# Performance work log

Measured on AMD Instinct MI355X. Metric: run time of the kernel, lower is better.

## Reference

```python
import jax, jax.numpy as jnp
import numpy as np

N_NODES = 65536
N_EDGES = 1048576


def gcn_conv(x, edge_index, edge_weight, W, b):
    """PyG GCNConv: h = D^{-1/2}(A+I)D^{-1/2} x W + b, scatter to target (edge_index[1])."""
    n = x.shape[0]
    row, col = edge_index[0], edge_index[1]
    loop = jnp.arange(n)
    row_f = jnp.concatenate([row, loop])
    col_f = jnp.concatenate([col, loop])
    w_f = jnp.concatenate([edge_weight, jnp.ones((n,), dtype=x.dtype)])
    deg = jax.ops.segment_sum(w_f, col_f, num_segments=n)
    dis = jnp.where(deg > 0, jax.lax.rsqrt(jnp.where(deg > 0, deg, 1.0)), 0.0)
    norm = dis[row_f] * w_f * dis[col_f]  # [E+N]
    h = x @ W  # [N, out]
    msg = h[row_f] * norm[:, None]  # gather + scale
    out = jax.ops.segment_sum(msg, col_f, num_segments=n)
    return out + b


def setup_inputs() -> dict:
    key = jax.random.key(0)
    ks = jax.random.split(key, 8)
    x = jax.random.normal(ks[0], (N_NODES, 128), dtype=jnp.float32)
    edge_index = jax.random.randint(ks[1], (2, N_EDGES), 0, N_NODES, dtype=jnp.int64)
    edge_weight = jax.random.uniform(ks[2], (N_EDGES,), dtype=jnp.float32)
    W1 = jax.random.normal(ks[3], (128, 256), dtype=jnp.float32) * (128 ** -0.5)
    b1 = jnp.zeros((256,), dtype=jnp.float32)
    W2 = jax.random.normal(ks[4], (256, 128), dtype=jnp.float32) * (256 ** -0.5)
    b2 = jnp.zeros((128,), dtype=jnp.float32)
    W3 = jax.random.normal(ks[5], (128, 64), dtype=jnp.float32) * (128 ** -0.5)
    b3 = jnp.zeros((64,), dtype=jnp.float32)
    return {"x": x, "edge_index": edge_index, "edge_weight": edge_weight,
            "num_graphs": 64, "W1": W1, "b1": b1, "W2": W2, "b2": b2, "W3": W3, "b3": b3}


def reference(x, edge_index, edge_weight, num_graphs, W1, b1, W2, b2, W3, b3):
    h = jax.nn.relu(gcn_conv(x, edge_index, edge_weight, W1, b1))
    h = jax.nn.relu(gcn_conv(h, edge_index, edge_weight, W2, b2))
    h = gcn_conv(h, edge_index, edge_weight, W3, b3)  # [N, 64]
    g = h.reshape(num_graphs, -1, 64)
    pad = jnp.zeros((g.shape[0], 1, g.shape[2]), dtype=g.dtype)
    return jnp.concatenate([g, pad], axis=1)  # [num_graphs, nodes_per_graph+1, 64]
```

## Files before the change

### kernel.cpp

```cpp
#include <hip/hip_runtime.h>
#include <cstdint>

#define TPB 256

typedef __attribute__((ext_vector_type(8))) short bf16x8;
typedef __attribute__((ext_vector_type(4))) float f32x4;

__device__ inline unsigned short f2bf(float f) {
  unsigned u = __float_as_uint(f);
  u += 0x7fffu + ((u >> 16) & 1u);
  return (unsigned short)(u >> 16);
}
__device__ inline float bf2f(unsigned short h) {
  return __uint_as_float(((unsigned)h) << 16);
}

__device__ inline void gload_lds16(const void* g, void* l) {
  __builtin_amdgcn_global_load_lds(
      (const __attribute__((address_space(1))) unsigned int*)g,
      (__attribute__((address_space(3))) unsigned int*)l, 16, 0, 0);
}

__device__ inline void acc_bf8(float* acc, int4 raw, float nv) {
  acc[0] += nv * __uint_as_float(((unsigned)raw.x) << 16);
  acc[1] += nv * __uint_as_float(((unsigned)raw.x) & 0xffff0000u);
  acc[2] += nv * __uint_as_float(((unsigned)raw.y) << 16);
  acc[3] += nv * __uint_as_float(((unsigned)raw.y) & 0xffff0000u);
  acc[4] += nv * __uint_as_float(((unsigned)raw.z) << 16);
  acc[5] += nv * __uint_as_float(((unsigned)raw.z) & 0xffff0000u);
  acc[6] += nv * __uint_as_float(((unsigned)raw.w) << 16);
  acc[7] += nv * __uint_as_float(((unsigned)raw.w) & 0xffff0000u);
}


__global__ void k_x2bf(const float* __restrict__ x, unsigned short* __restrict__ xb,
                       long total8) {
  long i = blockIdx.x * (long)blockDim.x + threadIdx.x;
  if (i >= total8) return;
  const float4* p = reinterpret_cast<const float4*>(x + i * 8);
  float4 a = p[0], b = p[1];
  unsigned short h[8];
  h[0] = f2bf(a.x); h[1] = f2bf(a.y); h[2] = f2bf(a.z); h[3] = f2bf(a.w);
  h[4] = f2bf(b.x); h[5] = f2bf(b.y); h[6] = f2bf(b.z); h[7] = f2bf(b.w);
  *reinterpret_cast<int4*>(xb + i * 8) = *(int4*)h;
}


__global__ void k_count_deg8(const int* __restrict__ col, const float* __restrict__ w,
                             unsigned long long* __restrict__ pk8, int E, int n) {
  int e = blockIdx.x * blockDim.x + threadIdx.x;
  if (e >= E) return;
  int k = blockIdx.x & 7;
  int c = col[e];
  unsigned long long inc =
      (1ULL << 40) + (unsigned long long)(unsigned int)(w[e] * 4294967296.0f);
  atomicAdd(&pk8[(size_t)k * n + c], inc);
}

__global__ void k_decode8(const unsigned long long* __restrict__ pk8,
                          float* __restrict__ dis, int* __restrict__ cnt,
                          unsigned short* __restrict__ cum8, int n) {
  int i = blockIdx.x * blockDim.x + threadIdx.x;
  if (i >= n) return;
  unsigned long long tot = 0;
  int run = 0;
#pragma unroll
  for (int k = 0; k < 8; ++k) {
    unsigned long long v = pk8[(size_t)k * n + i];
    cum8[(size_t)k * n + i] = (unsigned short)run;
    run += (int)(v >> 40);
    tot += v & 0xFFFFFFFFFFULL;
  }
  cnt[i] = run;
  dis[i] = rsqrtf(1.0f + (float)tot * 2.3283064365386963e-10f);
}


__global__ void k_reduceA(const int* __restrict__ cnt, int* __restrict__ bsum) {
  __shared__ int s[256];
  int t = threadIdx.x;
  s[t] = cnt[blockIdx.x * 256 + t];
  __syncthreads();
  for (int st = 128; st > 0; st >>= 1) {
    if (t < st) s[t] += s[t + st];
    __syncthreads();
  }
  if (t == 0) bsum[blockIdx.x] = s[0];
}

__global__ void k_scanB(const int* __restrict__ bsum, int* __restrict__ boff) {
  __shared__ int s[256];
  int t = threadIdx.x;
  int v = bsum[t];
  s[t] = v;
  __syncthreads();
  for (int st = 1; st < 256; st <<= 1) {
    int a = (t >= st) ? s[t - st] : 0;
    __syncthreads();
    s[t] += a;
    __syncthreads();
  }
  boff[t] = s[t] - v;
}

__global__ void k_scanC(const int* __restrict__ cnt, const int* __restrict__ boff,
                        int* __restrict__ ptr, int n) {
  __shared__ int s[256];
  int t = threadIdx.x;
  int i = blockIdx.x * 256 + t;
  int v = cnt[i];
  s[t] = v;
  __syncthreads();
  for (int st = 1; st < 256; st <<= 1) {
    int a = (t >= st) ? s[t - st] : 0;
    __syncthreads();
    s[t] += a;
    __syncthreads();
  }
  int excl = boff[blockIdx.x] + s[t] - v;
  ptr[i] = excl;
  if (i == n - 1) ptr[n] = excl + v;
}

__global__ void k_cur8(const int* __restrict__ ptr, const unsigned short* __restrict__ cum8,
                       int* __restrict__ cur8, int n) {
  int i = blockIdx.x * blockDim.x + threadIdx.x;
  if (i >= n) return;
  int k = blockIdx.y;
  cur8[(size_t)k * n + i] = ptr[i] + cum8[(size_t)k * n + i];
}


__global__ void k_scatter_norm8(const int* __restrict__ row, const int* __restrict__ col,
                                const float* __restrict__ w, const float* __restrict__ dis,
                                int* __restrict__ cur8, int2* __restrict__ edat,
                                int E, int n) {
  int e = blockIdx.x * blockDim.x + threadIdx.x;
  if (e >= E) return;
  int k = blockIdx.x & 7;
  int c = col[e];
  int r = row[e];
  float nv = dis[r] * w[e] * dis[c];
  int p = atomicAdd(&cur8[(size_t)k * n + c], 1);
  edat[p] = make_int2(r, __float_as_int(nv));
}


__device__ inline void wprep_one(const float* __restrict__ W, unsigned short* __restrict__ Fh,
                                 unsigned short* __restrict__ Fl, int t, int M) {
  int l = t & 63;
  int rest = t >> 6;
  int nt16 = M >> 4;
  int c0t = rest % nt16;
  int ks = rest / nt16;
  int colg = c0t * 16 + (l & 15);
  int krow = (ks << 5) + ((l >> 4) << 3);
  size_t ob = (size_t)t * 8;
#pragma unroll
  for (int j = 0; j < 8; ++j) {
    float f = W[(size_t)(krow + j) * M + colg];
    unsigned short h = f2bf(f);
    Fh[ob + j] = h;
    Fl[ob + j] = f2bf(f - bf2f(h));
  }
}

__global__ void k_wprep3(const float* __restrict__ W1, const float* __restrict__ W2,
                         const float* __restrict__ W3,
                         unsigned short* __restrict__ f1h, unsigned short* __restrict__ f1l,
                         unsigned short* __restrict__ f2h, unsigned short* __restrict__ f2l,
                         unsigned short* __restrict__ f3h, unsigned short* __restrict__ f3l) {
  int t = blockIdx.x * blockDim.x + threadIdx.x;
  if (t < 4096) wprep_one(W1, f1h, f1l, t, 256);
  else if (t < 8192) wprep_one(W2, f2h, f2l, t - 4096, 128);
  else if (t < 9216) wprep_one(W3, f3h, f3l, t - 8192, 64);
}


template<int GL, bool RELU, bool BIAS>
__global__ __launch_bounds__(256) void k_gagg(const int* __restrict__ ptr,
                                              const int2* __restrict__ edat,
                                              const unsigned short* __restrict__ src,
                                              const float* __restrict__ dis,
                                              const float* __restrict__ bias,
                                              unsigned short* __restrict__ outp, int n) {
  constexpr int F = GL * 8;
  constexpr int GPB = 256 / GL;
  const int gid = blockIdx.x * GPB + threadIdx.x / GL;
  const int lane = threadIdx.x % GL;
  if (gid >= n) return;
  const int e0 = ptr[gid], e1 = ptr[gid + 1];
  float d = dis[gid];
  float ss = d * d;
  float acc[8] = {0.f, 0.f, 0.f, 0.f, 0.f, 0.f, 0.f, 0.f};
  {
    int4 raw = *reinterpret_cast<const int4*>(src + (size_t)gid * F + lane * 8);
    acc_bf8(acc, raw, ss);
  }
  int e = e0;
  for (; e + 8 <= e1; e += 8) {
    int2 ed[8];
#pragma unroll
    for (int u = 0; u < 8; ++u) ed[u] = edat[e + u];
    int4 raw[8];
#pragma unroll
    for (int u = 0; u < 8; ++u)
      raw[u] = *reinterpret_cast<const int4*>(src + (size_t)ed[u].x * F + lane * 8);
#pragma unroll
    for (int u = 0; u < 8; ++u) acc_bf8(acc, raw[u], __int_as_float(ed[u].y));
  }
  for (; e + 4 <= e1; e += 4) {
    int2 ed[4];
#pragma unroll
    for (int u = 0; u < 4; ++u) ed[u] = edat[e + u];
    int4 raw[4];
#pragma unroll
    for (int u = 0; u < 4; ++u)
      raw[u] = *reinterpret_cast<const int4*>(src + (size_t)ed[u].x * F + lane * 8);
#pragma unroll
    for (int u = 0; u < 4; ++u) acc_bf8(acc, raw[u], __int_as_float(ed[u].y));
  }
  for (; e < e1; ++e) {
    int2 ed = edat[e];
    int4 raw = *reinterpret_cast<const int4*>(src + (size_t)ed.x * F + lane * 8);
    acc_bf8(acc, raw, __int_as_float(ed.y));
  }
  if (BIAS) {
#pragma unroll
    for (int j = 0; j < 8; ++j) acc[j] += bias[lane * 8 + j];
  }
  if (RELU) {
#pragma unroll
    for (int j = 0; j < 8; ++j) acc[j] = fmaxf(acc[j], 0.f);
  }
  unsigned short hv[8];
#pragma unroll
  for (int j = 0; j < 8; ++j) hv[j] = f2bf(acc[j]);
  *reinterpret_cast<int4*>(outp + (size_t)gid * F + lane * 8) = *(int4*)hv;
}

__global__ __launch_bounds__(256) void k_gagg_out(const int* __restrict__ ptr,
                                                  const int2* __restrict__ edat,
                                                  const unsigned short* __restrict__ t3,
                                                  const float* __restrict__ dis,
                                                  const float* __restrict__ b3,
                                                  float* __restrict__ out,
                                                  const int* __restrict__ ngp,
                                                  int n, int nrows) {
  const int gid = blockIdx.x * 32 + threadIdx.x / 8;
  const int lane = threadIdx.x % 8;
  if (gid >= nrows) return;
  const int ng = *ngp;
  const int npg = n / ng;
  const int g = gid / (npg + 1);
  const int r = gid - g * (npg + 1);
  float acc[8] = {0.f, 0.f, 0.f, 0.f, 0.f, 0.f, 0.f, 0.f};
  if (r < npg) {
    const int i = g * npg + r;
    const int e0 = ptr[i], e1 = ptr[i + 1];
    float d = dis[i];
    float ss = d * d;
    int4 sraw = *reinterpret_cast<const int4*>(t3 + (size_t)i * 64 + lane * 8);
    acc_bf8(acc, sraw, ss);
    int e = e0;
    for (; e + 8 <= e1; e += 8) {
      int2 ed[8];
#pragma unroll
      for (int u = 0; u < 8; ++u) ed[u] = edat[e + u];
      int4 raw[8];
#pragma unroll
      for (int u = 0; u < 8; ++u)
        raw[u] = *reinterpret_cast<const int4*>(t3 + (size_t)ed[u].x * 64 + lane * 8);
#pragma unroll
      for (int u = 0; u < 8; ++u) acc_bf8(acc, raw[u], __int_as_float(ed[u].y));
    }
    for (; e + 4 <= e1; e += 4) {
      int2 ed[4];
#pragma unroll
      for (int u = 0; u < 4; ++u) ed[u] = edat[e + u];
      int4 raw[4];
#pragma unroll
      for (int u = 0; u < 4; ++u)
        raw[u] = *reinterpret_cast<const int4*>(t3 + (size_t)ed[u].x * 64 + lane * 8);
#pragma unroll
      for (int u = 0; u < 4; ++u) acc_bf8(acc, raw[u], __int_as_float(ed[u].y));
    }
    for (; e < e1; ++e) {
      int2 ed = edat[e];
      int4 raw = *reinterpret_cast<const int4*>(t3 + (size_t)ed.x * 64 + lane * 8);
      acc_bf8(acc, raw, __int_as_float(ed.y));
    }
#pragma unroll
    for (int j = 0; j < 8; ++j) acc[j] += b3[lane * 8 + j];
  }
  float4 o0 = make_float4(acc[0], acc[1], acc[2], acc[3]);
  float4 o1 = make_float4(acc[4], acc[5], acc[6], acc[7]);
  *reinterpret_cast<float4*>(out + (size_t)gid * 64 + lane * 8) = o0;
  *reinterpret_cast<float4*>(out + (size_t)gid * 64 + lane * 8 + 4) = o1;
}


template<bool BIAS, bool RELU>
__global__ __launch_bounds__(256) void gemm_mfma(
    const unsigned short* __restrict__ A,
    const unsigned short* __restrict__ BfHi, const unsigned short* __restrict__ BfLo,
    const float* __restrict__ bias,
    unsigned short* __restrict__ C, int K, int M) {
  __shared__ unsigned short AL[4096];
  const int tid = threadIdx.x;
  const int l = tid & 63;
  const int w = tid >> 6;
  const int m0 = blockIdx.x * 128;
  const int wmt = (w >> 1) * 4;
  const int wn = (w & 1) * 2;
  const int ntile0 = blockIdx.y * 4 + wn;
  const int nt16 = M >> 4;

  f32x4 acc[4][2];
#pragma unroll
  for (int a = 0; a < 4; ++a)
#pragma unroll
    for (int b = 0; b < 2; ++b) acc[a][b] = f32x4{0.f, 0.f, 0.f, 0.f};

  const int nks = K >> 5;
  for (int ks = 0; ks < nks; ++ks) {
    if (ks) __syncthreads();
#pragma unroll
    for (int rr = 0; rr < 2; ++rr) {
      int s = rr * 256 + tid;
      int mt = s >> 6, sl = s & 63;
      size_t grow = (size_t)(m0 + mt * 16 + (sl & 15)) * K + (ks << 5) + ((sl >> 4) << 3);
      gload_lds16(A + grow, &AL[(size_t)s * 8]);
    }
    int4 braw[2][2];
#pragma unroll
    for (int nt = 0; nt < 2; ++nt) {
      size_t bidx = ((size_t)(ks * nt16 + ntile0 + nt) * 64 + l) * 8;
      braw[nt][0] = *reinterpret_cast<const int4*>(BfHi + bidx);
      braw[nt][1] = *reinterpret_cast<const int4*>(BfLo + bidx);
    }
    asm volatile("s_waitcnt vmcnt(0)" ::: "memory");
    __syncthreads();
#pragma unroll
    for (int mt = 0; mt < 4; ++mt) {
      int slot = (wmt + mt) * 64 + l;
      bf16x8 av = __builtin_bit_cast(bf16x8, *reinterpret_cast<const int4*>(&AL[(size_t)slot * 8]));
#pragma unroll
      for (int nt = 0; nt < 2; ++nt) {
        bf16x8 bh = __builtin_bit_cast(bf16x8, braw[nt][0]);
        bf16x8 bl = __builtin_bit_cast(bf16x8, braw[nt][1]);
        acc[mt][nt] = __builtin_amdgcn_mfma_f32_16x16x32_bf16(av, bl, acc[mt][nt], 0, 0, 0);
        acc[mt][nt] = __builtin_amdgcn_mfma_f32_16x16x32_bf16(av, bh, acc[mt][nt], 0, 0, 0);
      }
    }
  }
#pragma unroll
  for (int mt = 0; mt < 4; ++mt) {
    int rowb = m0 + (wmt + mt) * 16 + ((l >> 4) << 2);
#pragma unroll
    for (int nt = 0; nt < 2; ++nt) {
      int colg = (ntile0 + nt) * 16 + (l & 15);
      float bv = 0.f;
      if (BIAS) bv = bias[colg];
#pragma unroll
      for (int i = 0; i < 4; ++i) {
        float v = acc[mt][nt][i] + bv;
        if (RELU) v = fmaxf(v, 0.f);
        C[(size_t)(rowb + i) * M + colg] = f2bf(v);
      }
    }
  }
}


static inline int nblk(long work, int tpb = TPB) { return (int)((work + tpb - 1) / tpb); }

extern "C" void kernel_launch(void* const* d_in, const int* in_sizes, int n_in,
                              void* d_out, int out_size, void* d_ws, size_t ws_size,
                              hipStream_t stream) {
  const float* x  = (const float*)d_in[0];
  const int*   ei = (const int*)d_in[1];
  const float* ew = (const float*)d_in[2];
  const int*  ngp = (const int*)d_in[3];
  const float* W1 = (const float*)d_in[4];
  const float* b1 = (const float*)d_in[5];
  const float* W2 = (const float*)d_in[6];
  const float* b2 = (const float*)d_in[7];
  const float* W3 = (const float*)d_in[8];
  const float* b3 = (const float*)d_in[9];
  float* out = (float*)d_out;

  const int n = in_sizes[0] / 128;
  const int E = in_sizes[2];
  const int* row = ei;
  const int* col = ei + E;

  const size_t MB = 1024 * 1024;
  char* W8 = (char*)d_ws;
  int2* edat = (int2*)W8;
  unsigned long long* pk8 = (unsigned long long*)(W8 + 8 * MB);
  int* cnt   = (int*)(W8 + 12 * MB);
  int* ptrv  = cnt + n;
  int* bsum  = ptrv + n + 1;
  int* boff  = bsum + 256;
  float* dis = (float*)(boff + 256);
  unsigned short* cum8 = (unsigned short*)(dis + n);
  int* cur8  = (int*)(cum8 + 8 * (size_t)n);
  unsigned short* xb  = (unsigned short*)(W8 + 16 * MB);
  unsigned short* t1u = (unsigned short*)(W8 + 32 * MB);
  unsigned short* t2u = (unsigned short*)(W8 + 32 * MB);
  unsigned short* t3u = (unsigned short*)(W8 + 32 * MB);
  unsigned short* h1u = (unsigned short*)(W8 + 48 * MB);
  unsigned short* h2u = (unsigned short*)(W8 + 48 * MB);
  unsigned short* w1fh = (unsigned short*)(W8 + 80 * MB);
  unsigned short* w1fl = w1fh + 32768;
  unsigned short* w2fh = w1fl + 32768;
  unsigned short* w2fl = w2fh + 32768;
  unsigned short* w3fh = w2fl + 32768;
  unsigned short* w3fl = w3fh + 8192;

  hipMemsetAsync(pk8, 0, (size_t)n * 8 * 8, stream);
  k_x2bf<<<nblk((long)n * 16), TPB, 0, stream>>>(x, xb, (long)n * 16);
  k_count_deg8<<<nblk(E), TPB, 0, stream>>>(col, ew, pk8, E, n);
  k_decode8<<<nblk(n), TPB, 0, stream>>>(pk8, dis, cnt, cum8, n);
  k_reduceA<<<n / 256, 256, 0, stream>>>(cnt, bsum);
  k_scanB<<<1, 256, 0, stream>>>(bsum, boff);
  k_scanC<<<n / 256, 256, 0, stream>>>(cnt, boff, ptrv, n);
  {
    dim3 g(nblk(n), 8);
    k_cur8<<<g, TPB, 0, stream>>>(ptrv, cum8, cur8, n);
  }
  k_scatter_norm8<<<nblk(E), TPB, 0, stream>>>(row, col, ew, dis, cur8, edat, E, n);

  k_wprep3<<<nblk(9216), TPB, 0, stream>>>(W1, W2, W3, w1fh, w1fl, w2fh, w2fl, w3fh, w3fl);

  k_gagg<16, false, false><<<nblk((long)n * 16), TPB, 0, stream>>>(
      ptrv, edat, xb, dis, nullptr, t1u, n);
  {
    dim3 g(n / 128, 256 / 64);
    gemm_mfma<true, true><<<g, 256, 0, stream>>>(t1u, w1fh, w1fl, b1, h1u, 128, 256);
  }

  {
    dim3 g(n / 128, 128 / 64);
    gemm_mfma<false, false><<<g, 256, 0, stream>>>(h1u, w2fh, w2fl, nullptr, t2u, 256, 128);
  }
  k_gagg<16, true, true><<<nblk((long)n * 16), TPB, 0, stream>>>(
      ptrv, edat, t2u, dis, b2, h2u, n);

  {
    dim3 g(n / 128, 64 / 64);
    gemm_mfma<false, false><<<g, 256, 0, stream>>>(h2u, w3fh, w3fl, nullptr, t3u, 128, 64);
  }
  const int nrows = out_size / 64;
  k_gagg_out<<<nblk((long)nrows * 8), TPB, 0, stream>>>(
      ptrv, edat, t3u, dis, b3, out, ngp, n, nrows);
}
```

Baseline: 373.3 us.

## Build CSR via two-pass coarse binning instead of per-node atomics and scans

Replaces the per-node 64-bit atomic degree count, multi-kernel prefix scan and global per-node cursor scatter with a two-level bucket sort. Edges are first binned into 1024 coarse bins of 64 nodes using a few contended global atomics. Per-bin blocks then compute degree, dis and local offsets with LDS atomics and write the final CSR edge data. This is meant to cut global atomic traffic, the 8x-node cursor arrays and launch count, at the cost of an extra pass over a temporary edge buffer. Row is packed into 16 bits, so node ids must stay below 65536. Degree summation now uses float atomics, so the result is no longer deterministic.

```diff
diff --git a/kernel.cpp b/kernel.cpp
--- a/kernel.cpp
+++ b/kernel.cpp
@@ -46,103 +46,107 @@
 }
 
 
-__global__ void k_count_deg8(const int* __restrict__ col, const float* __restrict__ w,
-                             unsigned long long* __restrict__ pk8, int E, int n) {
+__global__ void k_bincnt(const int* __restrict__ col, int* __restrict__ bcnt8, int E) {
+  int e = blockIdx.x * blockDim.x + threadIdx.x;
+  if (e >= E) return;
+  int k = blockIdx.x & 7;
+  atomicAdd(&bcnt8[k * 1024 + (col[e] >> 6)], 1);
+}
+
+__global__ void k_binscan(const int* __restrict__ bcnt8, int* __restrict__ base8,
+                          int* __restrict__ binstart, int* __restrict__ ptrv, int n) {
+  __shared__ int psum[256];
+  int t = threadIdx.x;
+  int loc = 0;
+  for (int b = t * 4; b < t * 4 + 4; ++b)
+#pragma unroll
+    for (int k = 0; k < 8; ++k) loc += bcnt8[k * 1024 + b];
+  psum[t] = loc;
+  __syncthreads();
+  for (int st = 1; st < 256; st <<= 1) {
+    int a = (t >= st) ? psum[t - st] : 0;
+    __syncthreads();
+    psum[t] += a;
+    __syncthreads();
+  }
+  int run = psum[t] - loc;
+  for (int b = t * 4; b < t * 4 + 4; ++b) {
+    binstart[b] = run;
+#pragma unroll
+    for (int k = 0; k < 8; ++k) {
+      base8[k * 1024 + b] = run;
+      run += bcnt8[k * 1024 + b];
+    }
+  }
+  if (t == 255) { binstart[1024] = run; ptrv[n] = run; }
+}
+
+__global__ void k_binscatter(const int* __restrict__ row, const int* __restrict__ col,
+                             const float* __restrict__ w, int* __restrict__ bcur8,
+                             int2* __restrict__ tmp, int E) {
   int e = blockIdx.x * blockDim.x + threadIdx.x;
   if (e >= E) return;
   int k = blockIdx.x & 7;
   int c = col[e];
-  unsigned long long inc =
-      (1ULL << 40) + (unsigned long long)(unsigned int)(w[e] * 4294967296.0f);
-  atomicAdd(&pk8[(size_t)k * n + c], inc);
-}
-
-__global__ void k_decode8(const unsigned long long* __restrict__ pk8,
-                          float* __restrict__ dis, int* __restrict__ cnt,
-                          unsigned short* __restrict__ cum8, int n) {
-  int i = blockIdx.x * blockDim.x + threadIdx.x;
-  if (i >= n) return;
-  unsigned long long tot = 0;
-  int run = 0;
-#pragma unroll
-  for (int k = 0; k < 8; ++k) {
-    unsigned long long v = pk8[(size_t)k * n + i];
-    cum8[(size_t)k * n + i] = (unsigned short)run;
-    run += (int)(v >> 40);
-    tot += v & 0xFFFFFFFFFFULL;
-  }
-  cnt[i] = run;
-  dis[i] = rsqrtf(1.0f + (float)tot * 2.3283064365386963e-10f);
-}
-
-
-__global__ void k_reduceA(const int* __restrict__ cnt, int* __restrict__ bsum) {
-  __shared__ int s[256];
-  int t = threadIdx.x;
-  s[t] = cnt[blockIdx.x * 256 + t];
+  int p = atomicAdd(&bcur8[k * 1024 + (c >> 6)], 1);
+  tmp[p] = make_int2(row[e] | ((c & 63) << 16), __float_as_int(w[e]));
+}
+
+__global__ __launch_bounds__(256) void k_pass2a(const int2* __restrict__ tmp,
+                                                const int* __restrict__ binstart,
+                                                int* __restrict__ ptrv,
+                                                float* __restrict__ dis) {
+  __shared__ int lcnt[64];
+  __shared__ float ldeg[64];
+  __shared__ int loff[64];
+  const int b = blockIdx.x;
+  const int t = threadIdx.x;
+  if (t < 64) { lcnt[t] = 0; ldeg[t] = 0.f; }
   __syncthreads();
-  for (int st = 128; st > 0; st >>= 1) {
-    if (t < st) s[t] += s[t + st];
-    __syncthreads();
-  }
-  if (t == 0) bsum[blockIdx.x] = s[0];
-}
-
-__global__ void k_scanB(const int* __restrict__ bsum, int* __restrict__ boff) {
-  __shared__ int s[256];
-  int t = threadIdx.x;
-  int v = bsum[t];
-  s[t] = v;
+  const int s = binstart[b], epn = binstart[b + 1];
+  for (int i = s + t; i < epn; i += 256) {
+    int2 d = tmp[i];
+    int lc = (d.x >> 16) & 63;
+    atomicAdd(&lcnt[lc], 1);
+    atomicAdd(&ldeg[lc], __int_as_float(d.y));
+  }
   __syncthreads();
-  for (int st = 1; st < 256; st <<= 1) {
-    int a = (t >= st) ? s[t - st] : 0;
-    __syncthreads();
-    s[t] += a;
-    __syncthreads();
-  }
-  boff[t] = s[t] - v;
-}
-
-__global__ void k_scanC(const int* __restrict__ cnt, const int* __restrict__ boff,
-                        int* __restrict__ ptr, int n) {
-  __shared__ int s[256];
-  int t = threadIdx.x;
-  int i = blockIdx.x * 256 + t;
-  int v = cnt[i];
-  s[t] = v;
+  if (t == 0) {
+    int r = 0;
+    for (int j = 0; j < 64; ++j) { loff[j] = r; r += lcnt[j]; }
+  }
   __syncthreads();
-  for (int st = 1; st < 256; st <<= 1) {
-    int a = (t >= st) ? s[t - st] : 0;
-    __syncthreads();
-    s[t] += a;
-    __syncthreads();
-  }
-  int excl = boff[blockIdx.x] + s[t] - v;
-  ptr[i] = excl;
-  if (i == n - 1) ptr[n] = excl + v;
-}
-
-__global__ void k_cur8(const int* __restrict__ ptr, const unsigned short* __restrict__ cum8,
-                       int* __restrict__ cur8, int n) {
-  int i = blockIdx.x * blockDim.x + threadIdx.x;
-  if (i >= n) return;
-  int k = blockIdx.y;
-  cur8[(size_t)k * n + i] = ptr[i] + cum8[(size_t)k * n + i];
-}
-
-
-__global__ void k_scatter_norm8(const int* __restrict__ row, const int* __restrict__ col,
-                                const float* __restrict__ w, const float* __restrict__ dis,
-                                int* __restrict__ cur8, int2* __restrict__ edat,
-                                int E, int n) {
-  int e = blockIdx.x * blockDim.x + threadIdx.x;
-  if (e >= E) return;
-  int k = blockIdx.x & 7;
-  int c = col[e];
-  int r = row[e];
-  float nv = dis[r] * w[e] * dis[c];
-  int p = atomicAdd(&cur8[(size_t)k * n + c], 1);
-  edat[p] = make_int2(r, __float_as_int(nv));
+  if (t < 64) {
+    int node = b * 64 + t;
+    ptrv[node] = s + loff[t];
+    dis[node] = rsqrtf(1.0f + ldeg[t]);
+  }
+}
+
+__global__ __launch_bounds__(256) void k_pass2b(const int2* __restrict__ tmp,
+                                                const int* __restrict__ binstart,
+                                                const int* __restrict__ ptrv,
+                                                const float* __restrict__ dis,
+                                                int2* __restrict__ edat) {
+  __shared__ int lcur[64];
+  __shared__ float ldis[64];
+  const int b = blockIdx.x;
+  const int t = threadIdx.x;
+  if (t < 64) {
+    int node = b * 64 + t;
+    lcur[t] = ptrv[node];
+    ldis[t] = dis[node];
+  }
+  __syncthreads();
+  const int s = binstart[b], epn = binstart[b + 1];
+  for (int i = s + t; i < epn; i += 256) {
+    int2 d = tmp[i];
+    int r = d.x & 0xFFFF;
+    int lc = (d.x >> 16) & 63;
+    float nv = dis[r] * __int_as_float(d.y) * ldis[lc];
+    int p = atomicAdd(&lcur[lc], 1);
+    edat[p] = make_int2(r, __float_as_int(nv));
+  }
 }
 
 
@@ -398,39 +402,32 @@
   const size_t MB = 1024 * 1024;
   char* W8 = (char*)d_ws;
   int2* edat = (int2*)W8;
-  unsigned long long* pk8 = (unsigned long long*)(W8 + 8 * MB);
-  int* cnt   = (int*)(W8 + 12 * MB);
-  int* ptrv  = cnt + n;
-  int* bsum  = ptrv + n + 1;
-  int* boff  = bsum + 256;
-  float* dis = (float*)(boff + 256);
-  unsigned short* cum8 = (unsigned short*)(dis + n);
-  int* cur8  = (int*)(cum8 + 8 * (size_t)n);
-  unsigned short* xb  = (unsigned short*)(W8 + 16 * MB);
-  unsigned short* t1u = (unsigned short*)(W8 + 32 * MB);
-  unsigned short* t2u = (unsigned short*)(W8 + 32 * MB);
-  unsigned short* t3u = (unsigned short*)(W8 + 32 * MB);
-  unsigned short* h1u = (unsigned short*)(W8 + 48 * MB);
-  unsigned short* h2u = (unsigned short*)(W8 + 48 * MB);
-  unsigned short* w1fh = (unsigned short*)(W8 + 80 * MB);
+  int2* tmp  = (int2*)(W8 + 8 * MB);
+  int* bcnt8 = (int*)(W8 + 16 * MB);
+  int* base8 = bcnt8 + 8192;
+  int* binstart = base8 + 8192;
+  int* ptrv  = binstart + 1025 + 3;
+  float* dis = (float*)(ptrv + n + 1);
+  unsigned short* xb  = (unsigned short*)(W8 + 17 * MB);
+  unsigned short* t1u = (unsigned short*)(W8 + 33 * MB);
+  unsigned short* t2u = t1u;
+  unsigned short* t3u = t1u;
+  unsigned short* h1u = (unsigned short*)(W8 + 49 * MB);
+  unsigned short* h2u = h1u;
+  unsigned short* w1fh = (unsigned short*)(W8 + 81 * MB);
   unsigned short* w1fl = w1fh + 32768;
   unsigned short* w2fh = w1fl + 32768;
   unsigned short* w2fl = w2fh + 32768;
   unsigned short* w3fh = w2fl + 32768;
   unsigned short* w3fl = w3fh + 8192;
 
-  hipMemsetAsync(pk8, 0, (size_t)n * 8 * 8, stream);
+  hipMemsetAsync(bcnt8, 0, 8192 * sizeof(int), stream);
   k_x2bf<<<nblk((long)n * 16), TPB, 0, stream>>>(x, xb, (long)n * 16);
-  k_count_deg8<<<nblk(E), TPB, 0, stream>>>(col, ew, pk8, E, n);
-  k_decode8<<<nblk(n), TPB, 0, stream>>>(pk8, dis, cnt, cum8, n);
-  k_reduceA<<<n / 256, 256, 0, stream>>>(cnt, bsum);
-  k_scanB<<<1, 256, 0, stream>>>(bsum, boff);
-  k_scanC<<<n / 256, 256, 0, stream>>>(cnt, boff, ptrv, n);
-  {
-    dim3 g(nblk(n), 8);
-    k_cur8<<<g, TPB, 0, stream>>>(ptrv, cum8, cur8, n);
-  }
-  k_scatter_norm8<<<nblk(E), TPB, 0, stream>>>(row, col, ew, dis, cur8, edat, E, n);
+  k_bincnt<<<nblk(E), TPB, 0, stream>>>(col, bcnt8, E);
+  k_binscan<<<1, 256, 0, stream>>>(bcnt8, base8, binstart, ptrv, n);
+  k_binscatter<<<nblk(E), TPB, 0, stream>>>(row, col, ew, base8, tmp, E);
+  k_pass2a<<<1024, 256, 0, stream>>>(tmp, binstart, ptrv, dis);
+  k_pass2b<<<1024, 256, 0, stream>>>(tmp, binstart, ptrv, dis, edat);
 
   k_wprep3<<<nblk(9216), TPB, 0, stream>>>(W1, W2, W3, w1fh, w1fl, w2fh, w2fl, w3fh, w3fl);
 
```

Result: no change. 379.6 us (+1.7%).
